# Kernel optimization log

Hardware: AMD Instinct MI355X
Metric: run time of the kernel (lower is better)

## Reference

```python
import jax, jax.numpy as jnp
import numpy as np

V, T, DA, DS, KR, DU, KA = 64, 8192, 256, 256, 8, 64, 40
BETA_DET = 1.0
EPS = 1e-8


def _l2n(x):
    # torch F.normalize: x / max(||x||_2, 1e-12) along last dim
    n = jnp.linalg.norm(x, axis=-1, keepdims=True)
    return x / jnp.maximum(n, 1e-12)


def setup_inputs() -> dict:
    key = jax.random.key(0)
    ks = jax.random.split(key, 10)
    f32 = jnp.float32
    return {
        "h_aligned": jax.random.normal(ks[0], (V, T, DA), f32),
        "alpha": jax.random.uniform(ks[1], (V,), f32),
        "pi": jax.random.uniform(ks[2], (KR,), f32),
        "US": jax.random.normal(ks[3], (KR * DU,), f32),
        "Wc_w": 0.02 * jax.random.normal(ks[4], (DS, KR * DU), f32),
        "Wc_b": jnp.zeros((DS,), f32),
        "Ws_w": 0.02 * jax.random.normal(ks[5], (DS, KR * DU), f32),
        "Ws_b": jnp.zeros((DS,), f32),
        "det_w": 0.02 * jax.random.normal(ks[6], (1, DS), f32),
        "det_b": jnp.zeros((1,), f32),
        "cls_w": 0.02 * jax.random.normal(ks[7], (KA, DS), f32),
        "cls_b": jnp.zeros((KA,), f32),
        "Wwin_w": 0.02 * jax.random.normal(ks[8], (DS, DA), f32),
        "tau_c0": jnp.zeros((), f32),
        "lamU": jnp.asarray(0.1, f32),
        "lamC": jnp.asarray(0.1, f32),
        "lamP": jnp.asarray(0.1, f32),
        "lamPi": jnp.asarray(0.1, f32),
        "nu": jnp.zeros((), f32),
        "risk": jnp.zeros((), f32),
    }


def reference(h_aligned, alpha, pi, US, Wc_w, Wc_b, Ws_w, Ws_b, det_w, det_b,
              cls_w, cls_b, Wwin_w, tau_c0, lamU, lamC, lamP, lamPi, nu, risk):
    # SCD small heads
    zc = US @ Wc_w.T + Wc_b            # (ds,) -- computed as in original (unused downstream)
    zs = US @ Ws_w.T + Ws_b            # (ds,)
    s = zs @ det_w[0] + det_b[0]       # scalar detection score

    # tau_x from entropies
    C_alpha = 1.0 - (-(alpha * jnp.log(alpha + EPS)).sum()) / jnp.log(jnp.asarray(float(V), alpha.dtype))
    u_pi = (-(pi * jnp.log(pi + EPS)).sum()) / jnp.log(jnp.asarray(float(KR), pi.dtype))
    tau_x = tau_c0 - lamU * nu - lamC * C_alpha + lamP * risk + lamPi * u_pi

    p_det = jax.nn.sigmoid(BETA_DET * (s - tau_x))
    y_hat = jax.nn.sigmoid(zs @ cls_w.T + cls_b)   # (Ka,)

    # qpl_localize: per-window cosine score against normalized zs
    z_win = _l2n(jnp.einsum('vtd,sd->vts', h_aligned, Wwin_w))  # (V,T,ds)
    e = jnp.einsum('vts,s->vt', z_win, _l2n(zs))                # (V,T)
    E_view = e.mean(axis=1)                                     # (V,)
    r_view = -0.5 * alpha                                       # r0=0, beta_alpha=0.5

    # vectorized run-length interval detection (replaces python V*T loop):
    # starts[v,t]=True iff an interval begins at t; ends[v,t]=True iff one ends at t
    I = e >= r_view[:, None]                                    # (V,T) bool
    prev = jnp.pad(I[:, :-1], ((0, 0), (1, 0)))
    nxt = jnp.pad(I[:, 1:], ((0, 0), (0, 1)))
    starts = I & ~prev
    ends = I & ~nxt

    I_view = E_view >= r_view
    flag_unknown = (p_det >= 0.5) & (~I_view.any())
    return (p_det, tau_x, y_hat, e, E_view, r_view, I_view, starts, ends, flag_unknown)
```

## Files before the change

### kernel.cpp

```cpp
#include <hip/hip_runtime.h>
#include <math.h>

#define V 64
#define T 8192
#define DA 256
#define DS 256
#define KR 8
#define KA 40
#define KRDU 512

#define OUT_PDET   0
#define OUT_TAU    1
#define OUT_YHAT   2
#define OUT_E      42
#define OUT_EVIEW  524330
#define OUT_RVIEW  524394
#define OUT_IVIEW  524458
#define OUT_STARTS 524522
#define OUT_ENDS   1048810
#define OUT_FLAG   1573098

#define WS_W    0
#define WS_ESUM 256
#define WS_ZSN  320
#define WS_CNT  576
#define WS_LIST 640

#define CAP    65536
#define MARGIN 4e-3f
#define HROWB  264

typedef __attribute__((ext_vector_type(8))) short short8;
typedef __attribute__((ext_vector_type(4))) float f32x4;

__device__ __forceinline__ unsigned pack_bf16(float a, float b) {
    union { float f; unsigned u; } x, y; x.f = a; y.f = b;
    unsigned ua = (x.u + 0x7FFFu + ((x.u >> 16) & 1u)) >> 16;
    unsigned ub = (y.u + 0x7FFFu + ((y.u >> 16) & 1u)) & 0xFFFF0000u;
    return ua | ub;
}

__global__ __launch_bounds__(256) void head_kernel(
    const float* __restrict__ alpha, const float* __restrict__ pi,
    const float* __restrict__ US, const float* __restrict__ Ws_w,
    const float* __restrict__ Ws_b, const float* __restrict__ det_w,
    const float* __restrict__ det_b, const float* __restrict__ cls_w,
    const float* __restrict__ cls_b,
    const float* __restrict__ tau_c0, const float* __restrict__ lamU,
    const float* __restrict__ lamC, const float* __restrict__ lamP,
    const float* __restrict__ lamPi, const float* __restrict__ nu,
    const float* __restrict__ risk,
    float* __restrict__ out, float* __restrict__ ws, int* __restrict__ wsi)
{
    __shared__ float us[KRDU];
    __shared__ float zs[DS];
    __shared__ float red[256];
    const int tid = threadIdx.x;
    const int rr = tid >> 4;
    const int c  = tid & 15;

    us[tid]       = US[tid];
    us[tid + 256] = US[tid + 256];
    __syncthreads();

    for (int rg = 0; rg < 16; ++rg) {
        int row = rg * 16 + rr;
        const float4* wr = (const float4*)(Ws_w + (size_t)row * KRDU);
        float a = 0.0f;
        #pragma unroll
        for (int jj = 0; jj < 8; ++jj) {
            float4 w4 = wr[jj * 16 + c];
            int j0 = (jj * 16 + c) * 4;
            a += w4.x * us[j0] + w4.y * us[j0+1] + w4.z * us[j0+2] + w4.w * us[j0+3];
        }
        #pragma unroll
        for (int m = 8; m >= 1; m >>= 1) a += __shfl_xor(a, m);
        if (c == 0) zs[row] = a;
    }
    __syncthreads();
    float zv = zs[tid] + Ws_b[tid];
    __syncthreads();
    zs[tid] = zv;

    red[tid] = zv * det_w[tid];
    __syncthreads();
    for (int off = 128; off > 0; off >>= 1) { if (tid < off) red[tid] += red[tid+off]; __syncthreads(); }
    float s_det = red[0] + det_b[0];
    __syncthreads();

    red[tid] = zv * zv;
    __syncthreads();
    for (int off = 128; off > 0; off >>= 1) { if (tid < off) red[tid] += red[tid+off]; __syncthreads(); }
    float inv_n = 1.0f / fmaxf(sqrtf(red[0]), 1e-12f);
    __syncthreads();
    ws[WS_ZSN + tid] = zv * inv_n;

    float term = 0.0f;
    if (tid < V) { float a = alpha[tid]; term = -a * logf(a + 1e-8f); }
    red[tid] = term;
    __syncthreads();
    for (int off = 128; off > 0; off >>= 1) { if (tid < off) red[tid] += red[tid+off]; __syncthreads(); }
    float C_alpha = 1.0f - red[0] / logf((float)V);
    __syncthreads();

    term = 0.0f;
    if (tid < KR) { float p = pi[tid]; term = -p * logf(p + 1e-8f); }
    red[tid] = term;
    __syncthreads();
    for (int off = 128; off > 0; off >>= 1) { if (tid < off) red[tid] += red[tid+off]; __syncthreads(); }
    float u_pi = red[0] / logf((float)KR);
    __syncthreads();

    float tau = tau_c0[0] - lamU[0]*nu[0] - lamC[0]*C_alpha + lamP[0]*risk[0] + lamPi[0]*u_pi;
    if (tid == 0) {
        out[OUT_TAU]  = tau;
        out[OUT_PDET] = 1.0f / (1.0f + expf(-(s_det - tau)));
        wsi[WS_CNT]   = 0;
    }

    for (int rg = 0; rg < 3; ++rg) {
        int row = rg * 16 + rr;
        float a = 0.0f;
        if (row < KA) {
            const float4* cr4 = (const float4*)(cls_w + (size_t)row * DS);
            #pragma unroll
            for (int jj = 0; jj < 4; ++jj) {
                float4 w4 = cr4[jj * 16 + c];
                int j0 = (jj * 16 + c) * 4;
                a += w4.x * zs[j0] + w4.y * zs[j0+1] + w4.z * zs[j0+2] + w4.w * zs[j0+3];
            }
        }
        #pragma unroll
        for (int m = 8; m >= 1; m >>= 1) a += __shfl_xor(a, m);
        if (c == 0 && row < KA) out[OUT_YHAT + row] = 1.0f / (1.0f + expf(-(a + cls_b[row])));
    }

    ws[WS_W + tid] = 0.0f;
    if (tid < V) {
        out[OUT_RVIEW + tid] = -0.5f * alpha[tid];
        ws[WS_ESUM + tid] = 0.0f;
    }
}

__global__ __launch_bounds__(256) void wvec_kernel(const float* __restrict__ Wwin,
                                                   float* __restrict__ ws)
{
    __shared__ float zl[16];
    const int b = blockIdx.x;
    const int tid = threadIdx.x;
    if (tid < 16) zl[tid] = ws[WS_ZSN + b * 16 + tid];
    __syncthreads();
    float a = 0.0f;
    #pragma unroll
    for (int s = 0; s < 16; ++s) a += Wwin[(size_t)(b * 16 + s) * DA + tid] * zl[s];
    atomicAdd(&ws[WS_W + tid], a);
}

__global__ __launch_bounds__(256, 2) void escore_kernel(
    const float* __restrict__ h, const float* __restrict__ Wwin,
    const float* __restrict__ alpha,
    float* __restrict__ ws, int* __restrict__ wsi, float* __restrict__ out)
{
    __shared__ unsigned short hsb[2][16 * HROWB];
    __shared__ float part_n[4][1024];
    __shared__ float part_u[4][1024];
    __shared__ float red[4];

    const int tid  = threadIdx.x;
    const int lane = tid & 63;
    const int wv   = tid >> 6;
    const int ln15 = lane & 15;
    const int lq   = lane >> 4;

    short8 Wf[4][8];
    {
        const int nbase = wv * 64 + ln15;
        #pragma unroll
        for (int st = 0; st < 4; ++st) {
            const float* wrow = Wwin + (size_t)(nbase + st * 16) * DA + lq * 8;
            #pragma unroll
            for (int kk = 0; kk < 8; ++kk) {
                float4 f0 = *(const float4*)(wrow + kk * 32);
                float4 f1 = *(const float4*)(wrow + kk * 32 + 4);
                union { short8 s; unsigned u[4]; } pk;
                pk.u[0] = pack_bf16(f0.x, f0.y);
                pk.u[1] = pack_bf16(f0.z, f0.w);
                pk.u[2] = pack_bf16(f1.x, f1.y);
                pk.u[3] = pack_bf16(f1.z, f1.w);
                Wf[st][kk] = pk.s;
            }
        }
    }
    float zl[4];
    #pragma unroll
    for (int st = 0; st < 4; ++st) zl[st] = ws[WS_ZSN + wv * 64 + st * 16 + ln15];

    const int view = blockIdx.x >> 3;
    const float rv = -0.5f * alpha[view];
    const long rowbase0 = (long)blockIdx.x * 1024;

    float4 f[4];
    {
        const float4* hg = (const float4*)(h + rowbase0 * DA);
        #pragma unroll
        for (int i = 0; i < 4; ++i) f[i] = hg[tid + 256 * i];
    }

    for (int tile = 0; tile < 64; ++tile) {
        const int p = tile & 1;

        #pragma unroll
        for (int i = 0; i < 4; ++i) {
            unsigned u0 = pack_bf16(f[i].x, f[i].y);
            unsigned u1 = pack_bf16(f[i].z, f[i].w);
            *(uint2*)&hsb[p][(wv + 4 * i) * HROWB + lane * 4] = make_uint2(u0, u1);
        }
        __syncthreads();

        {
            int nt = (tile < 63) ? tile + 1 : 63;
            const float4* ng = (const float4*)(h + (rowbase0 + (long)nt * 16) * DA);
            #pragma unroll
            for (int i = 0; i < 4; ++i) f[i] = ng[tid + 256 * i];
        }

        f32x4 acc[4];
        #pragma unroll
        for (int st = 0; st < 4; ++st) acc[st] = (f32x4){0.f, 0.f, 0.f, 0.f};
        #pragma unroll
        for (int kk = 0; kk < 8; ++kk) {
            short8 af = *(const short8*)&hsb[p][ln15 * HROWB + kk * 32 + lq * 8];
            acc[0] = __builtin_amdgcn_mfma_f32_16x16x32_bf16(af, Wf[0][kk], acc[0], 0, 0, 0);
            acc[1] = __builtin_amdgcn_mfma_f32_16x16x32_bf16(af, Wf[1][kk], acc[1], 0, 0, 0);
            acc[2] = __builtin_amdgcn_mfma_f32_16x16x32_bf16(af, Wf[2][kk], acc[2], 0, 0, 0);
            acc[3] = __builtin_amdgcn_mfma_f32_16x16x32_bf16(af, Wf[3][kk], acc[3], 0, 0, 0);
        }

        float nr[4], nu[4];
        #pragma unroll
        for (int reg = 0; reg < 4; ++reg) {
            nr[reg] = acc[0][reg]*acc[0][reg] + acc[1][reg]*acc[1][reg]
                    + acc[2][reg]*acc[2][reg] + acc[3][reg]*acc[3][reg];
            nu[reg] = acc[0][reg]*zl[0] + acc[1][reg]*zl[1]
                    + acc[2][reg]*zl[2] + acc[3][reg]*zl[3];
        }
        #pragma unroll
        for (int m = 1; m <= 8; m <<= 1) {
            #pragma unroll
            for (int reg = 0; reg < 4; ++reg) {
                nr[reg] += __shfl_xor(nr[reg], m);
                nu[reg] += __shfl_xor(nu[reg], m);
            }
        }
        if (ln15 == 0) {
            *(float4*)&part_n[wv][tile * 16 + lq * 4] = make_float4(nr[0], nr[1], nr[2], nr[3]);
            *(float4*)&part_u[wv][tile * 16 + lq * 4] = make_float4(nu[0], nu[1], nu[2], nu[3]);
        }
    }
    __syncthreads();

    float esum = 0.0f;
    #pragma unroll
    for (int j = 0; j < 4; ++j) {
        int r = j * 256 + tid;
        float nn = part_n[0][r] + part_n[1][r] + part_n[2][r] + part_n[3][r];
        float uu = part_u[0][r] + part_u[1][r] + part_u[2][r] + part_u[3][r];
        float e = uu / fmaxf(sqrtf(nn), 1e-12f);
        out[OUT_E + rowbase0 + r] = e;
        esum += e;
        if (fabsf(e - rv) < MARGIN) {
            int idx = atomicAdd(&wsi[WS_CNT], 1);
            if (idx < CAP) wsi[WS_LIST + idx] = (int)(rowbase0 + r);
        }
    }
    #pragma unroll
    for (int m = 1; m <= 32; m <<= 1) esum += __shfl_xor(esum, m);
    if (lane == 0) red[wv] = esum;
    __syncthreads();
    if (tid == 0) atomicAdd(&ws[WS_ESUM + view], red[0] + red[1] + red[2] + red[3]);
}

__global__ __launch_bounds__(256) void fixup_kernel(
    const float* __restrict__ h, const float* __restrict__ Wwin,
    const float* __restrict__ alpha, const float* __restrict__ ws,
    const int* __restrict__ wsi, float* __restrict__ out)
{
    __shared__ float hrow[DA];
    __shared__ float red[8];
    const int tid  = threadIdx.x;
    const int lane = tid & 63;
    const int wv   = tid >> 6;
    const int cnt  = wsi[WS_CNT];
    const int m    = cnt < CAP ? cnt : CAP;

    for (int i = blockIdx.x; i < m; i += gridDim.x) {
        const int row = wsi[WS_LIST + i];
        hrow[tid] = h[(size_t)row * DA + tid];
        __syncthreads();
        const float4* wr = (const float4*)(Wwin + (size_t)tid * DA);
        const float4* h4 = (const float4*)hrow;
        float z0 = 0.f, z1 = 0.f, z2 = 0.f, z3 = 0.f;
        #pragma unroll 4
        for (int j = 0; j < 64; j += 4) {
            float4 a, b;
            a = wr[j];   b = h4[j];   z0 += a.x*b.x + a.y*b.y + a.z*b.z + a.w*b.w;
            a = wr[j+1]; b = h4[j+1]; z1 += a.x*b.x + a.y*b.y + a.z*b.z + a.w*b.w;
            a = wr[j+2]; b = h4[j+2]; z2 += a.x*b.x + a.y*b.y + a.z*b.z + a.w*b.w;
            a = wr[j+3]; b = h4[j+3]; z3 += a.x*b.x + a.y*b.y + a.z*b.z + a.w*b.w;
        }
        float zz  = (z0 + z1) + (z2 + z3);
        float nrm = zz * zz;
        float num = hrow[tid] * ws[WS_W + tid];
        #pragma unroll
        for (int s = 1; s <= 32; s <<= 1) { nrm += __shfl_xor(nrm, s); num += __shfl_xor(num, s); }
        if (lane == 0) { red[wv] = nrm; red[4 + wv] = num; }
        __syncthreads();
        if (tid == 0) {
            float nn = red[0] + red[1] + red[2] + red[3];
            float uu = red[4] + red[5] + red[6] + red[7];
            out[OUT_E + row] = uu / fmaxf(sqrtf(nn), 1e-12f);
        }
        __syncthreads();
    }

    if (cnt > CAP) {
        for (long i = blockIdx.x; i < (long)V * T; i += gridDim.x) {
            float r = -0.5f * alpha[i >> 13];
            if (fabsf(out[OUT_E + i] - r) >= MARGIN) continue;
            hrow[tid] = h[(size_t)i * DA + tid];
            __syncthreads();
            const float4* wr = (const float4*)(Wwin + (size_t)tid * DA);
            const float4* h4 = (const float4*)hrow;
            float z0 = 0.f, z1 = 0.f, z2 = 0.f, z3 = 0.f;
            for (int j = 0; j < 64; j += 4) {
                float4 a, b;
                a = wr[j];   b = h4[j];   z0 += a.x*b.x + a.y*b.y + a.z*b.z + a.w*b.w;
                a = wr[j+1]; b = h4[j+1]; z1 += a.x*b.x + a.y*b.y + a.z*b.z + a.w*b.w;
                a = wr[j+2]; b = h4[j+2]; z2 += a.x*b.x + a.y*b.y + a.z*b.z + a.w*b.w;
                a = wr[j+3]; b = h4[j+3]; z3 += a.x*b.x + a.y*b.y + a.z*b.z + a.w*b.w;
            }
            float zz  = (z0 + z1) + (z2 + z3);
            float nrm = zz * zz;
            float num = hrow[tid] * ws[WS_W + tid];
            for (int s = 1; s <= 32; s <<= 1) { nrm += __shfl_xor(nrm, s); num += __shfl_xor(num, s); }
            if (lane == 0) { red[wv] = nrm; red[4 + wv] = num; }
            __syncthreads();
            if (tid == 0) {
                float nn = red[0] + red[1] + red[2] + red[3];
                float uu = red[4] + red[5] + red[6] + red[7];
                out[OUT_E + i] = uu / fmaxf(sqrtf(nn), 1e-12f);
            }
            __syncthreads();
        }
    }
}

__global__ void finalize_kernel(const float* __restrict__ alpha,
                                const float* __restrict__ ws,
                                float* __restrict__ out)
{
    int v = threadIdx.x;
    float E = ws[WS_ESUM + v] * (1.0f / 8192.0f);
    out[OUT_EVIEW + v] = E;
    float r = -0.5f * alpha[v];
    bool Iv = (E >= r);
    out[OUT_IVIEW + v] = Iv ? 1.0f : 0.0f;
    unsigned long long bal = __ballot(Iv);
    if (v == 0) {
        float p = out[OUT_PDET];
        out[OUT_FLAG] = ((p >= 0.5f) && (bal == 0ULL)) ? 1.0f : 0.0f;
    }
}

__global__ __launch_bounds__(256) void intervals_kernel(
    const float* __restrict__ alpha, float* __restrict__ out)
{
    int idx = blockIdx.x * 256 + threadIdx.x;
    int v = idx >> 13;
    int t = idx & (T - 1);
    const float* e = out + OUT_E;
    float r = -0.5f * alpha[v];
    bool Ii = (e[idx] >= r);
    bool Ip = (t > 0)     && (e[idx - 1] >= r);
    bool In = (t < T - 1) && (e[idx + 1] >= r);
    out[OUT_STARTS + idx] = (Ii && !Ip) ? 1.0f : 0.0f;
    out[OUT_ENDS   + idx] = (Ii && !In) ? 1.0f : 0.0f;
}

extern "C" void kernel_launch(void* const* d_in, const int* in_sizes, int n_in,
                              void* d_out, int out_size, void* d_ws, size_t ws_size,
                              hipStream_t stream)
{
    const float* h      = (const float*)d_in[0];
    const float* alpha  = (const float*)d_in[1];
    const float* pi     = (const float*)d_in[2];
    const float* US     = (const float*)d_in[3];
    const float* Ws_w   = (const float*)d_in[6];
    const float* Ws_b   = (const float*)d_in[7];
    const float* det_w  = (const float*)d_in[8];
    const float* det_b  = (const float*)d_in[9];
    const float* cls_w  = (const float*)d_in[10];
    const float* cls_b  = (const float*)d_in[11];
    const float* Wwin   = (const float*)d_in[12];
    const float* tau_c0 = (const float*)d_in[13];
    const float* lamU   = (const float*)d_in[14];
    const float* lamC   = (const float*)d_in[15];
    const float* lamP   = (const float*)d_in[16];
    const float* lamPi  = (const float*)d_in[17];
    const float* nu     = (const float*)d_in[18];
    const float* risk   = (const float*)d_in[19];
    float* out = (float*)d_out;
    float* ws  = (float*)d_ws;
    int*   wsi = (int*)d_ws;

    head_kernel<<<1, 256, 0, stream>>>(alpha, pi, US, Ws_w, Ws_b, det_w, det_b,
                                       cls_w, cls_b, tau_c0, lamU, lamC,
                                       lamP, lamPi, nu, risk, out, ws, wsi);
    wvec_kernel<<<16, 256, 0, stream>>>(Wwin, ws);
    escore_kernel<<<512, 256, 0, stream>>>(h, Wwin, alpha, ws, wsi, out);
    fixup_kernel<<<512, 256, 0, stream>>>(h, Wwin, alpha, ws, wsi, out);
    finalize_kernel<<<1, 64, 0, stream>>>(alpha, ws, out);
    intervals_kernel<<<(V * T) / 256, 256, 0, stream>>>(alpha, out);
}
```

Measured before the change: 1.026 ms.

## Double-buffer h tile prefetch two ahead and fold finalize into intervals kernel

```diff
diff --git a/kernel.cpp b/kernel.cpp
--- a/kernel.cpp
+++ b/kernel.cpp
@@ -198,65 +198,78 @@
     const int view = blockIdx.x >> 3;
     const float rv = -0.5f * alpha[view];
     const long rowbase0 = (long)blockIdx.x * 1024;
-
-    float4 f[4];
-    {
-        const float4* hg = (const float4*)(h + rowbase0 * DA);
-        #pragma unroll
-        for (int i = 0; i < 4; ++i) f[i] = hg[tid + 256 * i];
-    }
-
-    for (int tile = 0; tile < 64; ++tile) {
-        const int p = tile & 1;
-
-        #pragma unroll
-        for (int i = 0; i < 4; ++i) {
-            unsigned u0 = pack_bf16(f[i].x, f[i].y);
-            unsigned u1 = pack_bf16(f[i].z, f[i].w);
-            *(uint2*)&hsb[p][(wv + 4 * i) * HROWB + lane * 4] = make_uint2(u0, u1);
-        }
+    const float4* hg = (const float4*)(h + rowbase0 * DA);
+
+    float4 fA[4], fB[4];
+    #pragma unroll
+    for (int i = 0; i < 4; ++i) fA[i] = hg[tid + 256 * i];
+    #pragma unroll
+    for (int i = 0; i < 4; ++i) fB[i] = hg[1024 + tid + 256 * i];
+
+#define STAGE(FREG, P)                                                          \
+    _Pragma("unroll")                                                           \
+    for (int i = 0; i < 4; ++i) {                                               \
+        unsigned u0 = pack_bf16(FREG[i].x, FREG[i].y);                          \
+        unsigned u1 = pack_bf16(FREG[i].z, FREG[i].w);                          \
+        *(uint2*)&hsb[P][(wv + 4 * i) * HROWB + lane * 4] = make_uint2(u0, u1); \
+    }
+
+#define LOADNEXT(FREG, TNEXT)                                                   \
+    if ((TNEXT) < 64) {                                                         \
+        const float4* ng = hg + (long)(TNEXT) * 1024;                           \
+        _Pragma("unroll")                                                       \
+        for (int i = 0; i < 4; ++i) FREG[i] = ng[tid + 256 * i];                \
+    }
+
+#define COMPUTE(P, TILE) {                                                              \
+    f32x4 acc0 = (f32x4){0.f,0.f,0.f,0.f}, acc1 = (f32x4){0.f,0.f,0.f,0.f};             \
+    f32x4 acc2 = (f32x4){0.f,0.f,0.f,0.f}, acc3 = (f32x4){0.f,0.f,0.f,0.f};             \
+    _Pragma("unroll")                                                                   \
+    for (int kk = 0; kk < 8; ++kk) {                                                    \
+        short8 af = *(const short8*)&hsb[P][ln15 * HROWB + kk * 32 + lq * 8];           \
+        acc0 = __builtin_amdgcn_mfma_f32_16x16x32_bf16(af, Wf[0][kk], acc0, 0, 0, 0);   \
+        acc1 = __builtin_amdgcn_mfma_f32_16x16x32_bf16(af, Wf[1][kk], acc1, 0, 0, 0);   \
+        acc2 = __builtin_amdgcn_mfma_f32_16x16x32_bf16(af, Wf[2][kk], acc2, 0, 0, 0);   \
+        acc3 = __builtin_amdgcn_mfma_f32_16x16x32_bf16(af, Wf[3][kk], acc3, 0, 0, 0);   \
+    }                                                                                   \
+    float nr[4], nu_[4];                                                                \
+    _Pragma("unroll")                                                                   \
+    for (int reg = 0; reg < 4; ++reg) {                                                 \
+        nr[reg]  = acc0[reg]*acc0[reg] + acc1[reg]*acc1[reg]                            \
+                 + acc2[reg]*acc2[reg] + acc3[reg]*acc3[reg];                           \
+        nu_[reg] = acc0[reg]*zl[0] + acc1[reg]*zl[1]                                    \
+                 + acc2[reg]*zl[2] + acc3[reg]*zl[3];                                   \
+    }                                                                                   \
+    _Pragma("unroll")                                                                   \
+    for (int m = 1; m <= 8; m <<= 1) {                                                  \
+        _Pragma("unroll")                                                               \
+        for (int reg = 0; reg < 4; ++reg) {                                             \
+            nr[reg]  += __shfl_xor(nr[reg], m);                                         \
+            nu_[reg] += __shfl_xor(nu_[reg], m);                                        \
+        }                                                                               \
+    }                                                                                   \
+    if (ln15 == 0) {                                                                    \
+        *(float4*)&part_n[wv][(TILE) * 16 + lq * 4] = make_float4(nr[0], nr[1], nr[2], nr[3]);      \
+        *(float4*)&part_u[wv][(TILE) * 16 + lq * 4] = make_float4(nu_[0], nu_[1], nu_[2], nu_[3]);  \
+    }                                                                                   \
+}
+
+    for (int it = 0; it < 32; ++it) {
+        const int t0 = it * 2;
+        STAGE(fA, 0)
+        LOADNEXT(fA, t0 + 2)
         __syncthreads();
-
-        {
-            int nt = (tile < 63) ? tile + 1 : 63;
-            const float4* ng = (const float4*)(h + (rowbase0 + (long)nt * 16) * DA);
-            #pragma unroll
-            for (int i = 0; i < 4; ++i) f[i] = ng[tid + 256 * i];
-        }
-
-        f32x4 acc[4];
-        #pragma unroll
-        for (int st = 0; st < 4; ++st) acc[st] = (f32x4){0.f, 0.f, 0.f, 0.f};
-        #pragma unroll
-        for (int kk = 0; kk < 8; ++kk) {
-            short8 af = *(const short8*)&hsb[p][ln15 * HROWB + kk * 32 + lq * 8];
-            acc[0] = __builtin_amdgcn_mfma_f32_16x16x32_bf16(af, Wf[0][kk], acc[0], 0, 0, 0);
-            acc[1] = __builtin_amdgcn_mfma_f32_16x16x32_bf16(af, Wf[1][kk], acc[1], 0, 0, 0);
-            acc[2] = __builtin_amdgcn_mfma_f32_16x16x32_bf16(af, Wf[2][kk], acc[2], 0, 0, 0);
-            acc[3] = __builtin_amdgcn_mfma_f32_16x16x32_bf16(af, Wf[3][kk], acc[3], 0, 0, 0);
-        }
-
-        float nr[4], nu[4];
-        #pragma unroll
-        for (int reg = 0; reg < 4; ++reg) {
-            nr[reg] = acc[0][reg]*acc[0][reg] + acc[1][reg]*acc[1][reg]
-                    + acc[2][reg]*acc[2][reg] + acc[3][reg]*acc[3][reg];
-            nu[reg] = acc[0][reg]*zl[0] + acc[1][reg]*zl[1]
-                    + acc[2][reg]*zl[2] + acc[3][reg]*zl[3];
-        }
-        #pragma unroll
-        for (int m = 1; m <= 8; m <<= 1) {
-            #pragma unroll
-            for (int reg = 0; reg < 4; ++reg) {
-                nr[reg] += __shfl_xor(nr[reg], m);
-                nu[reg] += __shfl_xor(nu[reg], m);
-            }
-        }
-        if (ln15 == 0) {
-            *(float4*)&part_n[wv][tile * 16 + lq * 4] = make_float4(nr[0], nr[1], nr[2], nr[3]);
-            *(float4*)&part_u[wv][tile * 16 + lq * 4] = make_float4(nu[0], nu[1], nu[2], nu[3]);
-        }
-    }
+        COMPUTE(0, t0)
+        STAGE(fB, 1)
+        LOADNEXT(fB, t0 + 3)
+        __syncthreads();
+        COMPUTE(1, t0 + 1)
+    }
+
+#undef STAGE
+#undef LOADNEXT
+#undef COMPUTE
+
     __syncthreads();
 
     float esum = 0.0f;
@@ -355,25 +368,9 @@
     }
 }
 
-__global__ void finalize_kernel(const float* __restrict__ alpha,
-                                const float* __restrict__ ws,
-                                float* __restrict__ out)
-{
-    int v = threadIdx.x;
-    float E = ws[WS_ESUM + v] * (1.0f / 8192.0f);
-    out[OUT_EVIEW + v] = E;
-    float r = -0.5f * alpha[v];
-    bool Iv = (E >= r);
-    out[OUT_IVIEW + v] = Iv ? 1.0f : 0.0f;
-    unsigned long long bal = __ballot(Iv);
-    if (v == 0) {
-        float p = out[OUT_PDET];
-        out[OUT_FLAG] = ((p >= 0.5f) && (bal == 0ULL)) ? 1.0f : 0.0f;
-    }
-}
-
 __global__ __launch_bounds__(256) void intervals_kernel(
-    const float* __restrict__ alpha, float* __restrict__ out)
+    const float* __restrict__ alpha, const float* __restrict__ ws,
+    float* __restrict__ out)
 {
     int idx = blockIdx.x * 256 + threadIdx.x;
     int v = idx >> 13;
@@ -385,6 +382,20 @@
     bool In = (t < T - 1) && (e[idx + 1] >= r);
     out[OUT_STARTS + idx] = (Ii && !Ip) ? 1.0f : 0.0f;
     out[OUT_ENDS   + idx] = (Ii && !In) ? 1.0f : 0.0f;
+
+    if (blockIdx.x == 0 && threadIdx.x < 64) {
+        int vv = threadIdx.x;
+        float E = ws[WS_ESUM + vv] * (1.0f / 8192.0f);
+        out[OUT_EVIEW + vv] = E;
+        float rr = -0.5f * alpha[vv];
+        bool Iv = (E >= rr);
+        out[OUT_IVIEW + vv] = Iv ? 1.0f : 0.0f;
+        unsigned long long bal = __ballot(Iv);
+        if (vv == 0) {
+            float p = out[OUT_PDET];
+            out[OUT_FLAG] = ((p >= 0.5f) && (bal == 0ULL)) ? 1.0f : 0.0f;
+        }
+    }
 }
 
 extern "C" void kernel_launch(void* const* d_in, const int* in_sizes, int n_in,
@@ -416,9 +427,8 @@
     head_kernel<<<1, 256, 0, stream>>>(alpha, pi, US, Ws_w, Ws_b, det_w, det_b,
                                        cls_w, cls_b, tau_c0, lamU, lamC,
                                        lamP, lamPi, nu, risk, out, ws, wsi);
+    escore_kernel<<<512, 256, 0, stream>>>(h, Wwin, alpha, ws, wsi, out);
     wvec_kernel<<<16, 256, 0, stream>>>(Wwin, ws);
-    escore_kernel<<<512, 256, 0, stream>>>(h, Wwin, alpha, ws, wsi, out);
     fixup_kernel<<<512, 256, 0, stream>>>(h, Wwin, alpha, ws, wsi, out);
-    finalize_kernel<<<1, 64, 0, stream>>>(alpha, ws, out);
-    intervals_kernel<<<(V * T) / 256, 256, 0, stream>>>(alpha, out);
-}
+    intervals_kernel<<<(V * T) / 256, 256, 0, stream>>>(alpha, ws, out);
+}
```

Result: no change. 1.014 ms (-1.2%).
